# Performance work log

Measured on AMD Instinct MI355X. Metric: run time of the kernel, lower is better.

## Reference

```python
import jax, jax.numpy as jnp
import numpy as np


def _ln(x, g, b, eps=1e-5):
    m = x.mean(-1, keepdims=True)
    v = ((x - m) ** 2).mean(-1, keepdims=True)
    return (x - m) * jax.lax.rsqrt(v + eps) * g + b


def setup_inputs() -> dict:
    key = jax.random.key(0)
    ks = jax.random.split(key, 12)
    B, S, I, H, E, P, O, EM = 32, 512, 64, 512, 8, 96, 64, 512
    D = S * I
    r = lambda k, shape, s=0.02: jax.random.normal(k, shape, jnp.float32) * s
    z = lambda *shape: jnp.zeros(shape, jnp.float32)
    o = lambda *shape: jnp.ones(shape, jnp.float32)
    return dict(
        x=jax.random.normal(ks[0], (B, S, I), jnp.float32),
        gW1=r(ks[1], (D, EM)), gb1=z(EM), gln1_g=o(EM), gln1_b=z(EM),
        gW2=r(ks[2], (EM, EM)), gb2=z(EM), gln2_g=o(EM), gln2_b=z(EM),
        gW3=r(ks[3], (EM, 128)), gb3=z(128),
        protos=jax.random.normal(ks[4], (E, 128), jnp.float32) * 0.01,
        temp=jnp.ones((), jnp.float32),
        eW1=r(ks[5], (E, I, H)), eb1=z(E, H),
        eW2=r(ks[6], (E, H, H)), eb2=z(E, H),
        fW1=r(ks[7], (H, H)), fb1=z(H), fln_g=o(H), fln_b=z(H),
        fW2=r(ks[8], (H, H)), fb2=z(H),
        ln_g=o(H), ln_b=z(H),
        pW1=r(ks[9], (H, H // 2)), pb1=z(H // 2), pln_g=o(H // 2), pln_b=z(H // 2),
        pW2=r(ks[10], (H // 2, P * O)), pb2=z(P * O),
        on_g=o(O), on_b=z(O),
    )


def reference(x, gW1, gb1, gln1_g, gln1_b, gW2, gb2, gln2_g, gln2_b, gW3, gb3,
              protos, temp, eW1, eb1, eW2, eb2,
              fW1, fb1, fln_g, fln_b, fW2, fb2, ln_g, ln_b,
              pW1, pb1, pln_g, pln_b, pW2, pb2, on_g, on_b):
    B, S, I = x.shape
    O = on_g.shape[0]
    P = pW2.shape[1] // O
    # 1) flow latent mapping (identity fallback path of the original code)
    x_flat = x.reshape(B, S * I)
    z_latent = x_flat
    # 2) gating encoder -> 128-d embedding (dropout = identity in eval)
    h = jax.nn.relu(_ln(z_latent @ gW1 + gb1, gln1_g, gln1_b))
    h = jax.nn.relu(_ln(h @ gW2 + gb2, gln2_g, gln2_b))
    emb = h @ gW3 + gb3  # [B, 128]
    # 3) routing: euclidean cdist to prototypes, temperature-scaled softmax
    d2 = jnp.sum((emb[:, None, :] - protos[None, :, :]) ** 2, axis=-1)
    dist = jnp.sqrt(jnp.maximum(d2, 1e-12))  # [B, E]
    t = jnp.clip(temp, 0.1, 5.0)
    w = jax.nn.softmax(-dist / t, axis=-1)  # [B, E]
    # 4) experts: per-expert FFN on raw input, all experts batched
    he = jax.nn.relu(jnp.einsum('bsi,eih->besh', x, eW1) + eb1[None, :, None, :])
    eo = jnp.einsum('besh,eho->beso', he, eW2) + eb2[None, :, None, :]  # [B,E,S,H]
    # 5) routing-weighted combine + fusion + prediction head
    fused = jnp.einsum('besh,be->bsh', eo, w)
    f = jax.nn.relu(_ln(fused @ fW1 + fb1, fln_g, fln_b)) @ fW2 + fb2
    f = _ln(f, ln_g, ln_b)
    last = f[:, -1, :]  # [B, H]
    p = jax.nn.relu(_ln(last @ pW1 + pb1, pln_g, pln_b)) @ pW2 + pb2
    p = p.reshape(B, P, O)
    return _ln(p, on_g, on_b)
```

## Files before the change

kernel.cpp:

```cpp
#include <hip/hip_runtime.h>
#include <math.h>

#define DIMK 32768

__device__ __forceinline__ void fma4(float4& a, float s, const float4 w) {
  a.x += s * w.x; a.y += s * w.y; a.z += s * w.z; a.w += s * w.w;
}

__device__ __forceinline__ float block_sum(float v, float* red, int n) {
  int t = threadIdx.x;
  red[t] = v;
  __syncthreads();
  for (int s = n >> 1; s > 0; s >>= 1) {
    if (t < s) red[t] += red[t + s];
    __syncthreads();
  }
  float r = red[0];
  __syncthreads();
  return r;
}

__global__ __launch_bounds__(256) void gemm1(const float* __restrict__ x,
                                             const float* __restrict__ gW1,
                                             float* __restrict__ part) {
  const int mt = blockIdx.x, ks = blockIdx.y;
  const int m0 = mt * 128, k0 = ks * 256;
  const int t = threadIdx.x;
  __shared__ float As[32 * 260];
  __shared__ float Ws[64 * 128];

  for (int i = t; i < 2048; i += 256) {
    int b = i >> 6, q = i & 63;
    *(float4*)&As[b * 260 + q * 4] = *(const float4*)(x + (size_t)b * DIMK + k0 + q * 4);
  }
  const float* Wp = gW1 + (size_t)k0 * 512 + m0;
  float4 wreg[8];
#pragma unroll
  for (int j = 0; j < 8; ++j) {
    int i = t + j * 256, r = i >> 5, q = i & 31;
    wreg[j] = *(const float4*)(Wp + (size_t)r * 512 + q * 4);
  }

  const int mf = t & 31, bg = t >> 5;
  const int b0 = bg * 4;
  float4 acc[4];
#pragma unroll
  for (int j = 0; j < 4; ++j) acc[j] = make_float4(0.f, 0.f, 0.f, 0.f);
  const float* a0 = &As[b0 * 260];

  for (int s = 0; s < 4; ++s) {
    __syncthreads();
#pragma unroll
    for (int j = 0; j < 8; ++j) {
      int i = t + j * 256, r = i >> 5, q = i & 31;
      *(float4*)&Ws[r * 128 + q * 4] = wreg[j];
    }
    __syncthreads();
    if (s < 3) {
      const float* Wn = Wp + (size_t)(s + 1) * 64 * 512;
#pragma unroll
      for (int j = 0; j < 8; ++j) {
        int i = t + j * 256, r = i >> 5, q = i & 31;
        wreg[j] = *(const float4*)(Wn + (size_t)r * 512 + q * 4);
      }
    }
    const float* ab = a0 + s * 64;
#pragma unroll 8
    for (int k = 0; k < 64; ++k) {
      float4 wv = *(const float4*)&Ws[k * 128 + mf * 4];
      float av0 = ab[k], av1 = ab[260 + k], av2 = ab[520 + k], av3 = ab[780 + k];
      fma4(acc[0], av0, wv);
      fma4(acc[1], av1, wv);
      fma4(acc[2], av2, wv);
      fma4(acc[3], av3, wv);
    }
  }

  float* op = part + ((size_t)ks * 32 + b0) * 512 + m0 + mf * 4;
#pragma unroll
  for (int j = 0; j < 4; ++j) *(float4*)(op + (size_t)j * 512) = acc[j];
}

__global__ __launch_bounds__(512) void gred_ln(const float* __restrict__ part,
                                               const float* __restrict__ gb1,
                                               const float* __restrict__ g, const float* __restrict__ bt,
                                               float* __restrict__ h1) {
  const int b = blockIdx.x, t = threadIdx.x;
  __shared__ float red[512];
  float a = gb1[t];
  const float* pp0 = part + (size_t)b * 512 + t;
#pragma unroll 8
  for (int ks = 0; ks < 128; ++ks) a += pp0[(size_t)ks * 16384];
  float mean = block_sum(a, red, 512) * (1.f / 512.f);
  float d = a - mean;
  float var = block_sum(d * d, red, 512) * (1.f / 512.f);
  h1[b * 512 + t] = fmaxf(d * rsqrtf(var + 1e-5f) * g[t] + bt[t], 0.f);
}

template <int KC>
__global__ __launch_bounds__(256) void gemm_tile(const float* __restrict__ A,
                                                 const float* __restrict__ W,
                                                 float* __restrict__ outp,
                                                 int M, int aRow,
                                                 size_t aStrideE, size_t wStrideE) {
  const int mt = blockIdx.x, kq = blockIdx.y, e = blockIdx.z, NE = gridDim.z;
  const int m0 = mt * 64, k0 = kq * KC;
  const int t = threadIdx.x;
  __shared__ float Ws[KC * 64];
  __shared__ float As[32 * (KC + 4)];
  const float* Wp = W + (size_t)e * wStrideE + (size_t)k0 * M + m0;
  for (int i = t; i < KC * 16; i += 256) {
    int r = i >> 4, q = i & 15;
    *(float4*)&Ws[r * 64 + q * 4] = *(const float4*)(Wp + (size_t)r * M + q * 4);
  }
  const float* Ap = A + (size_t)e * aStrideE + k0;
  for (int i = t; i < 32 * (KC / 4); i += 256) {
    int b = i / (KC / 4), q = i % (KC / 4);
    *(float4*)&As[b * (KC + 4) + q * 4] = *(const float4*)(Ap + (size_t)b * aRow + q * 4);
  }
  __syncthreads();
  const int mf = t & 15, bg = t >> 4;
  const int b0 = bg * 2;
  float4 acc0 = make_float4(0.f, 0.f, 0.f, 0.f), acc1 = acc0;
  const float* a0 = &As[b0 * (KC + 4)];
  const float* a1 = &As[(b0 + 1) * (KC + 4)];
#pragma unroll 8
  for (int k = 0; k < KC; ++k) {
    float4 wv = *(const float4*)&Ws[k * 64 + mf * 4];
    fma4(acc0, a0[k], wv);
    fma4(acc1, a1[k], wv);
  }
  float* op = outp + ((size_t)(kq * NE + e) * 32 + b0) * M + m0 + mf * 4;
  *(float4*)op = acc0;
  *(float4*)(op + M) = acc1;
}

__global__ void red_ln(const float* __restrict__ zp, const float* __restrict__ bias,
                       const float* __restrict__ g, const float* __restrict__ bt,
                       float* __restrict__ outp, int M, int nq, int relu) {
  const int b = blockIdx.x, t = threadIdx.x;
  __shared__ float red[512];
  float a = bias[t];
#pragma unroll 4
  for (int kq = 0; kq < nq; ++kq) a += zp[((size_t)kq * 32 + b) * M + t];
  float fM = 1.f / (float)M;
  float mean = block_sum(a, red, M) * fM;
  float d = a - mean;
  float var = block_sum(d * d, red, M) * fM;
  float v = d * rsqrtf(var + 1e-5f) * g[t] + bt[t];
  outp[b * M + t] = relu ? fmaxf(v, 0.f) : v;
}

__global__ __launch_bounds__(128) void gate_k(const float* __restrict__ zp2,
                                              const float* __restrict__ gb3,
                                              const float* __restrict__ protos,
                                              const float* __restrict__ temp,
                                              float* __restrict__ wgt) {
  __shared__ float red[128];
  __shared__ float d2s[8];
  const int b = blockIdx.x, t = threadIdx.x;
  float a = gb3[t];
#pragma unroll 4
  for (int kq = 0; kq < 16; ++kq) a += zp2[((size_t)kq * 32 + b) * 128 + t];
  for (int e = 0; e < 8; ++e) {
    float dd = a - protos[e * 128 + t];
    float s = block_sum(dd * dd, red, 128);
    if (t == 0) d2s[e] = s;
  }
  __syncthreads();
  if (t == 0) {
    float tt = fminf(fmaxf(temp[0], 0.1f), 5.0f);
    float lg[8], mx = -1e30f;
#pragma unroll
    for (int e = 0; e < 8; ++e) {
      float dist = sqrtf(fmaxf(d2s[e], 1e-12f));
      lg[e] = -dist / tt;
      mx = fmaxf(mx, lg[e]);
    }
    float se = 0.f;
#pragma unroll
    for (int e = 0; e < 8; ++e) { lg[e] = expf(lg[e] - mx); se += lg[e]; }
#pragma unroll
    for (int e = 0; e < 8; ++e) wgt[b * 8 + e] = lg[e] / se;
  }
}

__global__ __launch_bounds__(256) void he_k(const float* __restrict__ x,
                                            const float* __restrict__ eW1,
                                            const float* __restrict__ eb1,
                                            float* __restrict__ he_all) {
  const int e = blockIdx.x, hs = blockIdx.y;
  const int t = threadIdx.x;
  __shared__ float xs[32 * 64];
  __shared__ float Ws[64 * 256];
  for (int i = t; i < 512; i += 256) {
    int b = i >> 4, q = i & 15;
    *(float4*)&xs[b * 64 + q * 4] = *(const float4*)(x + (size_t)b * DIMK + 32704 + q * 4);
  }
  const float* w1 = eW1 + (size_t)e * 64 * 512 + hs * 256;
  for (int i = t; i < 64 * 64; i += 256) {
    int k = i >> 6, q = i & 63;
    *(float4*)&Ws[k * 256 + q * 4] = *(const float4*)(w1 + (size_t)k * 512 + q * 4);
  }
  __syncthreads();
  float acc[32];
#pragma unroll
  for (int b = 0; b < 32; ++b) acc[b] = 0.f;
#pragma unroll 4
  for (int k = 0; k < 64; ++k) {
    float wk = Ws[k * 256 + t];
#pragma unroll
    for (int b = 0; b < 32; ++b) acc[b] += xs[b * 64 + k] * wk;
  }
  float bb = eb1[e * 512 + hs * 256 + t];
  for (int b = 0; b < 32; ++b)
    he_all[((size_t)e * 32 + b) * 512 + hs * 256 + t] = fmaxf(acc[b] + bb, 0.f);
}

__global__ __launch_bounds__(512) void ffuse(const float* __restrict__ epart,
                                             const float* __restrict__ eb2,
                                             const float* __restrict__ wgt,
                                             float* __restrict__ fused) {
  const int b = blockIdx.x, t = threadIdx.x;
  __shared__ float wl[8];
  if (t < 8) wl[t] = wgt[b * 8 + t];
  __syncthreads();
  float a = 0.f;
#pragma unroll
  for (int e = 0; e < 8; ++e) {
    float s = eb2[e * 512 + t];
#pragma unroll
    for (int kq = 0; kq < 8; ++kq)
      s += epart[(((size_t)kq * 8 + e) * 32 + b) * 512 + t];
    a += wl[e] * s;
  }
  fused[b * 512 + t] = a;
}

__global__ __launch_bounds__(256) void fin_red(const float* __restrict__ fpart,
                                               const float* __restrict__ pb2,
                                               const float* __restrict__ ong,
                                               const float* __restrict__ onb,
                                               float* __restrict__ outp) {
  const int t = threadIdx.x;
  const int lane = t & 63, w = t >> 6;
  const int r = blockIdx.x * 4 + w;
  const int b = r / 96, pi = r % 96;
  const int m = pi * 64 + lane;
  float a = pb2[m];
#pragma unroll
  for (int kq = 0; kq < 8; ++kq) a += fpart[((size_t)kq * 32 + b) * 6144 + m];
  float s = a;
  s += __shfl_xor(s, 1); s += __shfl_xor(s, 2); s += __shfl_xor(s, 4);
  s += __shfl_xor(s, 8); s += __shfl_xor(s, 16); s += __shfl_xor(s, 32);
  float mean = s * (1.f / 64.f);
  float d = a - mean;
  float q = d * d;
  q += __shfl_xor(q, 1); q += __shfl_xor(q, 2); q += __shfl_xor(q, 4);
  q += __shfl_xor(q, 8); q += __shfl_xor(q, 16); q += __shfl_xor(q, 32);
  float rr = rsqrtf(q * (1.f / 64.f) + 1e-5f);
  outp[((size_t)b * 96 + pi) * 64 + lane] = d * rr * ong[lane] + onb[lane];
}

extern "C" void kernel_launch(void* const* d_in, const int* in_sizes, int n_in,
                              void* d_out, int out_size, void* d_ws, size_t ws_size,
                              hipStream_t stream) {
  (void)in_sizes; (void)n_in; (void)out_size; (void)ws_size;
  const float* x      = (const float*)d_in[0];
  const float* gW1    = (const float*)d_in[1];
  const float* gb1    = (const float*)d_in[2];
  const float* gln1_g = (const float*)d_in[3];
  const float* gln1_b = (const float*)d_in[4];
  const float* gW2    = (const float*)d_in[5];
  const float* gb2    = (const float*)d_in[6];
  const float* gln2_g = (const float*)d_in[7];
  const float* gln2_b = (const float*)d_in[8];
  const float* gW3    = (const float*)d_in[9];
  const float* gb3    = (const float*)d_in[10];
  const float* protos = (const float*)d_in[11];
  const float* temp   = (const float*)d_in[12];
  const float* eW1    = (const float*)d_in[13];
  const float* eb1    = (const float*)d_in[14];
  const float* eW2    = (const float*)d_in[15];
  const float* eb2    = (const float*)d_in[16];
  const float* fW1    = (const float*)d_in[17];
  const float* fb1    = (const float*)d_in[18];
  const float* fln_g  = (const float*)d_in[19];
  const float* fln_b  = (const float*)d_in[20];
  const float* fW2    = (const float*)d_in[21];
  const float* fb2    = (const float*)d_in[22];
  const float* ln_g   = (const float*)d_in[23];
  const float* ln_b   = (const float*)d_in[24];
  const float* pW1    = (const float*)d_in[25];
  const float* pb1    = (const float*)d_in[26];
  const float* pln_g  = (const float*)d_in[27];
  const float* pln_b  = (const float*)d_in[28];
  const float* pW2    = (const float*)d_in[29];
  const float* pb2    = (const float*)d_in[30];
  const float* on_g   = (const float*)d_in[31];
  const float* on_b   = (const float*)d_in[32];
  float* out = (float*)d_out;

  float* ws     = (float*)d_ws;
  float* part   = ws;
  float* epart  = ws;
  float* he_all = ws + 1048576;
  float* fpart  = ws;
  float* h1     = ws + 2097152;
  float* h2     = h1 + 16384;
  float* zp     = h2 + 16384;
  float* zp2    = zp + 262144;
  float* wgt    = zp2 + 65536;
  float* fused  = wgt + 256;
  float* f1     = fused + 16384;
  float* lastv  = f1 + 16384;
  float* pp     = lastv + 16384;

  gemm1<<<dim3(4, 128), 256, 0, stream>>>(x, gW1, part);
  gred_ln<<<32, 512, 0, stream>>>(part, gb1, gln1_g, gln1_b, h1);
  gemm_tile<32><<<dim3(8, 16, 1), 256, 0, stream>>>(h1, gW2, zp, 512, 512, 0, 0);
  red_ln<<<32, 512, 0, stream>>>(zp, gb2, gln2_g, gln2_b, h2, 512, 16, 1);
  gemm_tile<32><<<dim3(2, 16, 1), 256, 0, stream>>>(h2, gW3, zp2, 128, 512, 0, 0);
  gate_k<<<32, 128, 0, stream>>>(zp2, gb3, protos, temp, wgt);

  he_k<<<dim3(8, 2), 256, 0, stream>>>(x, eW1, eb1, he_all);
  gemm_tile<64><<<dim3(8, 8, 8), 256, 0, stream>>>(he_all, eW2, epart, 512, 512,
                                                   (size_t)32 * 512, (size_t)512 * 512);
  ffuse<<<32, 512, 0, stream>>>(epart, eb2, wgt, fused);

  gemm_tile<32><<<dim3(8, 16, 1), 256, 0, stream>>>(fused, fW1, zp, 512, 512, 0, 0);
  red_ln<<<32, 512, 0, stream>>>(zp, fb1, fln_g, fln_b, f1, 512, 16, 1);
  gemm_tile<32><<<dim3(8, 16, 1), 256, 0, stream>>>(f1, fW2, zp, 512, 512, 0, 0);
  red_ln<<<32, 512, 0, stream>>>(zp, fb2, ln_g, ln_b, lastv, 512, 16, 0);
  gemm_tile<32><<<dim3(4, 16, 1), 256, 0, stream>>>(lastv, pW1, zp, 256, 512, 0, 0);
  red_ln<<<32, 256, 0, stream>>>(zp, pb1, pln_g, pln_b, pp, 256, 16, 1);

  gemm_tile<32><<<dim3(96, 8, 1), 256, 0, stream>>>(pp, pW2, fpart, 6144, 256, 0, 0);
  fin_red<<<768, 256, 0, stream>>>(fpart, pb2, on_g, on_b, out);
}
```

Measured before the change: 298.7 us.

## Widen gemm1 tile to 256 columns with 8x4 register blocking

The gating GEMM1 kernel now covers 256 output columns per block instead of 128, and each thread computes an 8-row by 4-column register tile instead of 4x4. Activations are read from shared memory as float4 vectors over four k values, which cuts LDS instructions per FMA. The x slice is loaded once per block, so global reads of x are halved. In exchange the grid has half as many blocks (256), register use per thread rises, and the unpadded As stride may introduce bank conflicts.

Result: no change. 302.1 us (+1.1%).

```diff
diff --git a/kernel.cpp b/kernel.cpp
--- a/kernel.cpp
+++ b/kernel.cpp
@@ -5,6 +5,10 @@
 
 __device__ __forceinline__ void fma4(float4& a, float s, const float4 w) {
   a.x += s * w.x; a.y += s * w.y; a.z += s * w.z; a.w += s * w.w;
+}
+
+__device__ __forceinline__ float fsel(const float4& v, int kk) {
+  return kk == 0 ? v.x : kk == 1 ? v.y : kk == 2 ? v.z : v.w;
 }
 
 __device__ __forceinline__ float block_sum(float v, float* red, int n) {
@@ -24,61 +28,72 @@
                                              const float* __restrict__ gW1,
                                              float* __restrict__ part) {
   const int mt = blockIdx.x, ks = blockIdx.y;
-  const int m0 = mt * 128, k0 = ks * 256;
+  const int m0 = mt * 256, k0 = ks * 256;
   const int t = threadIdx.x;
-  __shared__ float As[32 * 260];
-  __shared__ float Ws[64 * 128];
-
-  for (int i = t; i < 2048; i += 256) {
-    int b = i >> 6, q = i & 63;
-    *(float4*)&As[b * 260 + q * 4] = *(const float4*)(x + (size_t)b * DIMK + k0 + q * 4);
+  __shared__ float As[32 * 256];
+  __shared__ float Ws[32 * 256];
+
+#pragma unroll
+  for (int j = 0; j < 8; ++j) {
+    int i = t + j * 256, b = i >> 6, q = i & 63;
+    *(float4*)&As[b * 256 + q * 4] = *(const float4*)(x + (size_t)b * DIMK + k0 + q * 4);
   }
   const float* Wp = gW1 + (size_t)k0 * 512 + m0;
   float4 wreg[8];
 #pragma unroll
   for (int j = 0; j < 8; ++j) {
-    int i = t + j * 256, r = i >> 5, q = i & 31;
+    int i = t + j * 256, r = i >> 6, q = i & 63;
     wreg[j] = *(const float4*)(Wp + (size_t)r * 512 + q * 4);
   }
 
-  const int mf = t & 31, bg = t >> 5;
-  const int b0 = bg * 4;
-  float4 acc[4];
-#pragma unroll
-  for (int j = 0; j < 4; ++j) acc[j] = make_float4(0.f, 0.f, 0.f, 0.f);
-  const float* a0 = &As[b0 * 260];
-
-  for (int s = 0; s < 4; ++s) {
+  const int mf4 = (t & 63) * 4;
+  const int bg = t >> 6;
+  float4 acc[8];
+#pragma unroll
+  for (int j = 0; j < 8; ++j) acc[j] = make_float4(0.f, 0.f, 0.f, 0.f);
+  const float* a0 = &As[bg * 8 * 256];
+
+  for (int s = 0; s < 8; ++s) {
     __syncthreads();
 #pragma unroll
     for (int j = 0; j < 8; ++j) {
-      int i = t + j * 256, r = i >> 5, q = i & 31;
-      *(float4*)&Ws[r * 128 + q * 4] = wreg[j];
+      int i = t + j * 256, r = i >> 6, q = i & 63;
+      *(float4*)&Ws[r * 256 + q * 4] = wreg[j];
     }
     __syncthreads();
-    if (s < 3) {
-      const float* Wn = Wp + (size_t)(s + 1) * 64 * 512;
+    if (s < 7) {
+      const float* Wn = Wp + (size_t)(s + 1) * 32 * 512;
 #pragma unroll
       for (int j = 0; j < 8; ++j) {
-        int i = t + j * 256, r = i >> 5, q = i & 31;
+        int i = t + j * 256, r = i >> 6, q = i & 63;
         wreg[j] = *(const float4*)(Wn + (size_t)r * 512 + q * 4);
       }
     }
-    const float* ab = a0 + s * 64;
-#pragma unroll 8
-    for (int k = 0; k < 64; ++k) {
-      float4 wv = *(const float4*)&Ws[k * 128 + mf * 4];
-      float av0 = ab[k], av1 = ab[260 + k], av2 = ab[520 + k], av3 = ab[780 + k];
-      fma4(acc[0], av0, wv);
-      fma4(acc[1], av1, wv);
-      fma4(acc[2], av2, wv);
-      fma4(acc[3], av3, wv);
+    const int sc = s * 32;
+#pragma unroll
+    for (int kq = 0; kq < 8; ++kq) {
+      float4 av[8];
+#pragma unroll
+      for (int bb = 0; bb < 8; ++bb)
+        av[bb] = *(const float4*)(a0 + bb * 256 + sc + kq * 4);
+#pragma unroll
+      for (int kk = 0; kk < 4; ++kk) {
+        float4 wv = *(const float4*)&Ws[(kq * 4 + kk) * 256 + mf4];
+        fma4(acc[0], fsel(av[0], kk), wv);
+        fma4(acc[1], fsel(av[1], kk), wv);
+        fma4(acc[2], fsel(av[2], kk), wv);
+        fma4(acc[3], fsel(av[3], kk), wv);
+        fma4(acc[4], fsel(av[4], kk), wv);
+        fma4(acc[5], fsel(av[5], kk), wv);
+        fma4(acc[6], fsel(av[6], kk), wv);
+        fma4(acc[7], fsel(av[7], kk), wv);
+      }
     }
   }
 
-  float* op = part + ((size_t)ks * 32 + b0) * 512 + m0 + mf * 4;
-#pragma unroll
-  for (int j = 0; j < 4; ++j) *(float4*)(op + (size_t)j * 512) = acc[j];
+  float* op = part + ((size_t)ks * 32 + bg * 8) * 512 + m0 + mf4;
+#pragma unroll
+  for (int j = 0; j < 8; ++j) *(float4*)(op + (size_t)j * 512) = acc[j];
 }
 
 __global__ __launch_bounds__(512) void gred_ln(const float* __restrict__ part,
@@ -316,7 +331,7 @@
   float* lastv  = f1 + 16384;
   float* pp     = lastv + 16384;
 
-  gemm1<<<dim3(4, 128), 256, 0, stream>>>(x, gW1, part);
+  gemm1<<<dim3(2, 128), 256, 0, stream>>>(x, gW1, part);
   gred_ln<<<32, 512, 0, stream>>>(part, gb1, gln1_g, gln1_b, h1);
   gemm_tile<32><<<dim3(8, 16, 1), 256, 0, stream>>>(h1, gW2, zp, 512, 512, 0, 0);
   red_ln<<<32, 512, 0, stream>>>(zp, gb2, gln2_g, gln2_b, h2, 512, 16, 1);
```
